# Optimization experiments

Hardware: AMD Instinct MI355X
Metric: run time of the kernel (lower is better)

Reference implementation:

```python
import jax, jax.numpy as jnp
import numpy as np

DET = 512       # detector bins
N_THETA = 180   # projection angles, theta = 0..179 degrees (1 deg spacing)


def _ramp_filter(size):
    """skimage _get_fourier_filter(size, 'ramp'): spatial ramp -> FFT."""
    n = np.concatenate((np.arange(1, size // 2 + 1, 2),
                        np.arange(size // 2 - 1, 0, -2)))
    f = np.zeros(size)
    f[0] = 0.25
    f[1::2] = -1.0 / (np.pi * n) ** 2
    return jnp.asarray(2.0 * np.real(np.fft.fft(f)), dtype=jnp.float32)


def _iradon(x):
    B, C, det, A = x.shape
    theta = jnp.deg2rad(jnp.arange(A, dtype=jnp.float32))  # 0..179 deg

    # --- ramp filtering along the detector axis ---
    size = max(64, int(2 ** np.ceil(np.log2(2 * det))))  # 1024 for det=512
    filt = _ramp_filter(size)                            # (size,)
    xp = jnp.pad(x, ((0, 0), (0, 0), (0, size - det), (0, 0)))
    proj_f = jnp.fft.fft(xp, axis=2) * filt[None, None, :, None]
    filtered = jnp.real(jnp.fft.ifft(proj_f, axis=2))[:, :, :det, :]  # (B,C,det,A)

    # --- backprojection (circle=False) ---
    out_size = int(np.floor(np.sqrt(det ** 2 / 2.0)))  # 362
    radius = out_size // 2
    xpr = jnp.arange(out_size, dtype=jnp.float32)[:, None] - radius  # rows
    ypr = jnp.arange(out_size, dtype=jnp.float32)[None, :] - radius  # cols
    cos_t = jnp.cos(theta)
    sin_t = jnp.sin(theta)
    # detector coordinate for every (angle, pixel): t = y*cos - x*sin
    t = ypr[None] * cos_t[:, None, None] - xpr[None] * sin_t[:, None, None]  # (A,out,out)
    pos = t + det // 2          # index into detector axis (x = arange(det)-det//2)
    i0 = jnp.floor(pos).astype(jnp.int32)
    frac = pos - i0.astype(jnp.float32)
    in_range = ((pos >= 0) & (pos <= det - 1)).astype(jnp.float32)  # fill_value=0 outside
    i0c = jnp.clip(i0, 0, det - 1)
    i1c = jnp.clip(i0 + 1, 0, det - 1)

    P = out_size * out_size
    ft = jnp.moveaxis(filtered, 3, 2)                     # (B,C,A,det)
    idx0 = jnp.broadcast_to(i0c.reshape(A, P)[None, None], (B, C, A, P))
    idx1 = jnp.broadcast_to(i1c.reshape(A, P)[None, None], (B, C, A, P))
    g0 = jnp.take_along_axis(ft, idx0, axis=3)            # (B,C,A,P)
    g1 = jnp.take_along_axis(ft, idx1, axis=3)
    w = frac.reshape(A, P)[None, None]
    m = in_range.reshape(A, P)[None, None]
    val = ((1.0 - w) * g0 + w * g1) * m                   # bilinear-in-1D interp, 0 outside
    recon = val.sum(axis=2).reshape(B, C, out_size, out_size)
    return recon * (jnp.pi / (2.0 * A))


def setup_inputs() -> dict:
    key = jax.random.key(0)
    x = jax.random.normal(key, (4, 1, DET, N_THETA), dtype=jnp.float32)
    return {"x": x}


def reference(x):
    return _iradon(x)
```

## Files before the change

### kernel.cpp

```cpp
#include <hip/hip_runtime.h>
#include <math.h>

#define DET 512
#define NA  180
#define OUT 362
#define RAD 181

#define NSPLIT 3
#define APB    60
#define CHUNK  10
#define LSTRIDE 516

constexpr double PI_D = 3.14159265358979323846;

constexpr double tsin(double x) {
    double x2 = x * x;
    return x * (1.0 + x2 * (-1.0/6 + x2 * (1.0/120 + x2 * (-1.0/5040 +
               x2 * (1.0/362880 + x2 * (-1.0/39916800))))));
}
constexpr double tcos(double x) {
    double x2 = x * x;
    return 1.0 + x2 * (-0.5 + x2 * (1.0/24 + x2 * (-1.0/720 +
               x2 * (1.0/40320 + x2 * (-1.0/3628800)))));
}

struct Trig { float c[NA]; float s[NA]; };
constexpr Trig make_trig() {
    Trig t{};
    constexpr double r = PI_D / 180.0;
    for (int k = 0; k < NA; ++k) {
        double c, s;
        if (k <= 45)       { c =  tcos(k * r);          s =  tsin(k * r); }
        else if (k <= 90)  { c =  tsin((90 - k) * r);   s =  tcos((90 - k) * r); }
        else if (k <= 135) { c = -tsin((k - 90) * r);   s =  tcos((k - 90) * r); }
        else               { c = -tcos((180 - k) * r);  s =  tsin((180 - k) * r); }
        t.c[k] = (float)c; t.s[k] = (float)s;
    }
    return t;
}
__device__ constexpr Trig TRIG = make_trig();

struct WTab { float w[2][127][8]; };
constexpr WTab make_wtab() {
    WTab t{};
    for (int h = 0; h < 2; ++h)
        for (int ui = 0; ui < 127; ++ui)
            for (int di = 0; di < 8; ++di) {
                int m = 8 * (ui - 63) + 2 * (di - 3) - 1 + 2 * h;
                double md = (double)m;
                t.w[h][ui][di] = (float)(-2.0 / (PI_D * PI_D * md * md));
            }
    return t;
}
__device__ constexpr WTab WTAB = make_wtab();

__global__ __launch_bounds__(128) void ramp_filter_kernel(
        const float* __restrict__ x, float* __restrict__ ft,
        float* __restrict__ out, int n4, int pb4) {
    const int a = blockIdx.x;
    const int b = blockIdx.y;
    const int t = threadIdx.x;

    {
        float4* oz = (float4*)out;
        const float4 z4 = make_float4(0.f, 0.f, 0.f, 0.f);
        const int base4 = (b * NA + a) * pb4;
        for (int i = t; i < pb4; i += 128) {
            int idx = base4 + i;
            if (idx < n4) oz[idx] = z4;
        }
    }

    __shared__ float Ef[768];
    __shared__ float Of[768];

    const float2 z2 = make_float2(0.f, 0.f);
    *(float2*)&Ef[2 * t]       = z2;
    *(float2*)&Ef[512 + 2 * t] = z2;
    *(float2*)&Of[2 * t]       = z2;
    *(float2*)&Of[512 + 2 * t] = z2;

    const float* xc = x + (size_t)(b * DET) * NA + a;
    float v0 = xc[(4 * t + 0) * NA];
    float v1 = xc[(4 * t + 1) * NA];
    float v2 = xc[(4 * t + 2) * NA];
    float v3 = xc[(4 * t + 3) * NA];
    *(float2*)&Ef[256 + 2 * t] = make_float2(v0, v2);
    *(float2*)&Of[256 + 2 * t] = make_float2(v1, v3);
    __syncthreads();

    const int half = t >> 6;
    const int tp   = t & 63;
    const float4* src4  = (const float4*)(half ? Ef : Of);
    const float4* self4 = (const float4*)(half ? Of : Ef);

    float acc0 = 0.f, acc1 = 0.f, acc2 = 0.f, acc3 = 0.f;
    #pragma unroll 4
    for (int ui = 0; ui < 127; ++ui) {
        const float* __restrict__ w = WTAB.w[half][ui];
        float4 s4 = src4[tp + (127 - ui)];
        acc0 = fmaf(s4.x, w[3], fmaf(s4.y, w[2], fmaf(s4.z, w[1], fmaf(s4.w, w[0], acc0))));
        acc1 = fmaf(s4.x, w[4], fmaf(s4.y, w[3], fmaf(s4.z, w[2], fmaf(s4.w, w[1], acc1))));
        acc2 = fmaf(s4.x, w[5], fmaf(s4.y, w[4], fmaf(s4.z, w[3], fmaf(s4.w, w[2], acc2))));
        acc3 = fmaf(s4.x, w[6], fmaf(s4.y, w[5], fmaf(s4.z, w[4], fmaf(s4.w, w[3], acc3))));
    }

    float4 sf = self4[64 + tp];
    acc0 = fmaf(0.5f, sf.x, acc0);
    acc1 = fmaf(0.5f, sf.y, acc1);
    acc2 = fmaf(0.5f, sf.z, acc2);
    acc3 = fmaf(0.5f, sf.w, acc3);

    float* o = ft + (b * NA + a) * DET + 8 * tp + half;
    o[0] = acc0;
    o[2] = acc1;
    o[4] = acc2;
    o[6] = acc3;
}

__device__ __forceinline__ float interp1(const float* __restrict__ L, float pos) {
    float pf = floorf(pos);
    int   i0 = (int)pf;
    float fr = pos - pf;
    float g0 = L[i0];
    float g1 = L[i0 + 1];
    float v  = fmaf(fr, g1 - g0, g0);
    return pos <= (float)(DET - 1) ? v : 0.0f;
}

__global__ __launch_bounds__(256) void backproject_kernel(
        const float* __restrict__ ft, float* __restrict__ out) {
    const int bz = blockIdx.z;
    const int b  = bz / NSPLIT;
    const int sp = bz - b * NSPLIT;
    const int r0 = blockIdx.y * 32;
    const int c0 = blockIdx.x * 32;
    const int tid = threadIdx.x;
    const int tx = tid & 15;
    const int ty = tid >> 4;

    __shared__ float line[CHUNK * LSTRIDE];

    if (tid < CHUNK) line[tid * LSTRIDE + 512] = 0.0f;

    const float xpr = (float)(min(r0 + ty, OUT - 1) - RAD);
    const float ypr = (float)(min(c0 + tx, OUT - 1) - RAD);

    float a00 = 0.0f, a01 = 0.0f, a10 = 0.0f, a11 = 0.0f;

    const float* base = ft + (b * NA + sp * APB) * DET;

    for (int rd = 0; rd < APB / CHUNK; ++rd) {
        __syncthreads();
        const float4* g = (const float4*)(base + rd * CHUNK * DET);
        #pragma unroll
        for (int k = 0; k < (CHUNK * DET / 4) / 256; ++k) {
            int j4 = tid + k * 256;
            float4 v = g[j4];
            int c = j4 >> 7;
            int d = (j4 & 127) << 2;
            *(float4*)&line[c * LSTRIDE + d] = v;
        }
        __syncthreads();

        const int abase = sp * APB + rd * CHUNK;
        #pragma unroll
        for (int i = 0; i < CHUNK; ++i) {
            const float cv = TRIG.c[abase + i];
            const float sv = TRIG.s[abase + i];
            float p00 = fmaf(ypr, cv, fmaf(xpr, -sv, 256.0f));
            float p01 = fmaf(16.0f, cv, p00);
            float p10 = fmaf(-16.0f, sv, p00);
            float p11 = fmaf(-16.0f, sv, p01);
            const float* L = line + i * LSTRIDE;
            a00 += interp1(L, p00);
            a01 += interp1(L, p01);
            a10 += interp1(L, p10);
            a11 += interp1(L, p11);
        }
    }

    const float scale = (float)(PI_D / (2.0 * NA));
    const int r = r0 + ty;
    const int c = c0 + tx;
    float* ob = out + b * OUT * OUT;
    if (r < OUT) {
        if (c < OUT)      atomicAdd(&ob[r * OUT + c],      a00 * scale);
        if (c + 16 < OUT) atomicAdd(&ob[r * OUT + c + 16], a01 * scale);
    }
    if (r + 16 < OUT) {
        if (c < OUT)      atomicAdd(&ob[(r + 16) * OUT + c],      a10 * scale);
        if (c + 16 < OUT) atomicAdd(&ob[(r + 16) * OUT + c + 16], a11 * scale);
    }
}

extern "C" void kernel_launch(void* const* d_in, const int* in_sizes, int n_in,
                              void* d_out, int out_size, void* d_ws, size_t ws_size,
                              hipStream_t stream) {
    const float* x = (const float*)d_in[0];
    float* ft  = (float*)d_ws;
    float* out = (float*)d_out;

    const int B = in_sizes[0] / (DET * NA);

    const int n4  = out_size / 4;
    const int pb4 = (n4 + NA * B - 1) / (NA * B);

    ramp_filter_kernel<<<dim3(NA, B), 128, 0, stream>>>(x, ft, out, n4, pb4);
    backproject_kernel<<<dim3((OUT + 31) / 32, (OUT + 31) / 32, B * NSPLIT),
                         256, 0, stream>>>(ft, out);
}
```

Measured before the change: 113.3 us.

## Store paired detector samples in LDS and stage filter weights in shared memory

The backprojection now stores each filtered projection in LDS as (g[i], g[i+1]) float2 pairs, so every interpolation needs one 64-bit LDS read instead of two scalar reads. The chunk size is halved to fit the doubled footprint, which doubles the number of barrier and reload rounds. The ramp filter copies its weight table into shared memory and reads it as float4 vectors instead of scalar constant-memory loads. It also remaps block indices to angles, interleaving angles across blocks.

```diff
diff --git a/kernel.cpp b/kernel.cpp
--- a/kernel.cpp
+++ b/kernel.cpp
@@ -8,8 +8,8 @@
 
 #define NSPLIT 3
 #define APB    60
-#define CHUNK  10
-#define LSTRIDE 516
+#define CHUNK  5
+#define PSTRIDE 514
 
 constexpr double PI_D = 3.14159265358979323846;
 
@@ -24,7 +24,7 @@
                x2 * (1.0/40320 + x2 * (-1.0/3628800)))));
 }
 
-struct Trig { float c[NA]; float s[NA]; };
+struct alignas(16) Trig { float c[NA]; float s[NA]; };
 constexpr Trig make_trig() {
     Trig t{};
     constexpr double r = PI_D / 180.0;
@@ -40,7 +40,7 @@
 }
 __device__ constexpr Trig TRIG = make_trig();
 
-struct WTab { float w[2][127][8]; };
+struct alignas(16) WTab { float w[2 * 127 * 8]; };
 constexpr WTab make_wtab() {
     WTab t{};
     for (int h = 0; h < 2; ++h)
@@ -48,7 +48,8 @@
             for (int di = 0; di < 8; ++di) {
                 int m = 8 * (ui - 63) + 2 * (di - 3) - 1 + 2 * h;
                 double md = (double)m;
-                t.w[h][ui][di] = (float)(-2.0 / (PI_D * PI_D * md * md));
+                t.w[(h * 127 + ui) * 8 + di] =
+                    (float)(-2.0 / (PI_D * PI_D * md * md));
             }
     return t;
 }
@@ -57,14 +58,17 @@
 __global__ __launch_bounds__(128) void ramp_filter_kernel(
         const float* __restrict__ x, float* __restrict__ ft,
         float* __restrict__ out, int n4, int pb4) {
-    const int a = blockIdx.x;
-    const int b = blockIdx.y;
-    const int t = threadIdx.x;
+    const int bx = blockIdx.x;
+    const int b  = blockIdx.y;
+    const int t  = threadIdx.x;
+
+    const int rr = bx & 7, qq = bx >> 3;
+    const int a  = 22 * rr + min(rr, 4) + qq;
 
     {
         float4* oz = (float4*)out;
         const float4 z4 = make_float4(0.f, 0.f, 0.f, 0.f);
-        const int base4 = (b * NA + a) * pb4;
+        const int base4 = (b * NA + bx) * pb4;
         for (int i = t; i < pb4; i += 128) {
             int idx = base4 + i;
             if (idx < n4) oz[idx] = z4;
@@ -73,6 +77,17 @@
 
     __shared__ float Ef[768];
     __shared__ float Of[768];
+    __shared__ float W[2 * 127 * 8];
+
+    {
+        const float4* wsrc = (const float4*)WTAB.w;
+        float4* wdst = (float4*)W;
+        #pragma unroll
+        for (int k = 0; k < 4; ++k) {
+            int i = t + k * 128;
+            if (i < 508) wdst[i] = wsrc[i];
+        }
+    }
 
     const float2 z2 = make_float2(0.f, 0.f);
     *(float2*)&Ef[2 * t]       = z2;
@@ -93,16 +108,18 @@
     const int tp   = t & 63;
     const float4* src4  = (const float4*)(half ? Ef : Of);
     const float4* self4 = (const float4*)(half ? Of : Ef);
+    const float*  Wh    = W + half * (127 * 8);
 
     float acc0 = 0.f, acc1 = 0.f, acc2 = 0.f, acc3 = 0.f;
-    #pragma unroll 4
+    #pragma unroll 2
     for (int ui = 0; ui < 127; ++ui) {
-        const float* __restrict__ w = WTAB.w[half][ui];
+        const float4 w0 = *(const float4*)&Wh[ui * 8];
+        const float4 w1 = *(const float4*)&Wh[ui * 8 + 4];
         float4 s4 = src4[tp + (127 - ui)];
-        acc0 = fmaf(s4.x, w[3], fmaf(s4.y, w[2], fmaf(s4.z, w[1], fmaf(s4.w, w[0], acc0))));
-        acc1 = fmaf(s4.x, w[4], fmaf(s4.y, w[3], fmaf(s4.z, w[2], fmaf(s4.w, w[1], acc1))));
-        acc2 = fmaf(s4.x, w[5], fmaf(s4.y, w[4], fmaf(s4.z, w[3], fmaf(s4.w, w[2], acc2))));
-        acc3 = fmaf(s4.x, w[6], fmaf(s4.y, w[5], fmaf(s4.z, w[4], fmaf(s4.w, w[3], acc3))));
+        acc0 = fmaf(s4.x, w0.w, fmaf(s4.y, w0.z, fmaf(s4.z, w0.y, fmaf(s4.w, w0.x, acc0))));
+        acc1 = fmaf(s4.x, w1.x, fmaf(s4.y, w0.w, fmaf(s4.z, w0.z, fmaf(s4.w, w0.y, acc1))));
+        acc2 = fmaf(s4.x, w1.y, fmaf(s4.y, w1.x, fmaf(s4.z, w0.w, fmaf(s4.w, w0.z, acc2))));
+        acc3 = fmaf(s4.x, w1.z, fmaf(s4.y, w1.y, fmaf(s4.z, w1.x, fmaf(s4.w, w0.w, acc3))));
     }
 
     float4 sf = self4[64 + tp];
@@ -118,13 +135,11 @@
     o[6] = acc3;
 }
 
-__device__ __forceinline__ float interp1(const float* __restrict__ L, float pos) {
+__device__ __forceinline__ float interp1(const float2* __restrict__ L, float pos) {
     float pf = floorf(pos);
-    int   i0 = (int)pf;
     float fr = pos - pf;
-    float g0 = L[i0];
-    float g1 = L[i0 + 1];
-    float v  = fmaf(fr, g1 - g0, g0);
+    float2 g = L[(int)pf];
+    float v  = fmaf(fr, g.y - g.x, g.x);
     return pos <= (float)(DET - 1) ? v : 0.0f;
 }
 
@@ -139,9 +154,7 @@
     const int tx = tid & 15;
     const int ty = tid >> 4;
 
-    __shared__ float line[CHUNK * LSTRIDE];
-
-    if (tid < CHUNK) line[tid * LSTRIDE + 512] = 0.0f;
+    __shared__ float2 pline[CHUNK][PSTRIDE];
 
     const float xpr = (float)(min(r0 + ty, OUT - 1) - RAD);
     const float ypr = (float)(min(c0 + tx, OUT - 1) - RAD);
@@ -152,14 +165,19 @@
 
     for (int rd = 0; rd < APB / CHUNK; ++rd) {
         __syncthreads();
-        const float4* g = (const float4*)(base + rd * CHUNK * DET);
+        const float* gsrc = base + rd * CHUNK * DET;
         #pragma unroll
-        for (int k = 0; k < (CHUNK * DET / 4) / 256; ++k) {
+        for (int k = 0; k < 3; ++k) {
             int j4 = tid + k * 256;
-            float4 v = g[j4];
-            int c = j4 >> 7;
-            int d = (j4 & 127) << 2;
-            *(float4*)&line[c * LSTRIDE + d] = v;
+            if (j4 < CHUNK * DET / 4) {
+                const float4 v = *(const float4*)&gsrc[j4 * 4];
+                int c = j4 >> 7;
+                int d = (j4 & 127) << 2;
+                float v4 = (d + 4 < DET) ? gsrc[j4 * 4 + 4] : 0.0f;
+                float2* dst = &pline[c][d];
+                *(float4*)&dst[0] = make_float4(v.x, v.y, v.y, v.z);
+                *(float4*)&dst[2] = make_float4(v.z, v.w, v.w, v4);
+            }
         }
         __syncthreads();
 
@@ -172,7 +190,7 @@
             float p01 = fmaf(16.0f, cv, p00);
             float p10 = fmaf(-16.0f, sv, p00);
             float p11 = fmaf(-16.0f, sv, p01);
-            const float* L = line + i * LSTRIDE;
+            const float2* L = pline[i];
             a00 += interp1(L, p00);
             a01 += interp1(L, p01);
             a10 += interp1(L, p10);
```

New measurement: 120.8 us. 6.6% more time.
